# Kernel optimization log

Measured on AMD Instinct MI355X. Metric: run time of the kernel, lower is better.

The kernel has to match this reference:

```python
import jax, jax.numpy as jnp
import numpy as np

MODES = 16
WIDTH = 64
DEPTH = 4
MLP = 128


def spectral_conv(x, w_cplx):
    # x: [B, C, H, W] float32; w_cplx: [C, C, m1, m2] complex64
    B, C, H, W = x.shape
    x_ft = jnp.fft.rfft2(x)  # [B, C, H, W//2+1] complex
    m1, m2 = MODES, MODES
    low = jnp.einsum('bixy,ioxy->boxy', x_ft[:, :, :m1, :m2], w_cplx)
    out_ft = jnp.zeros((B, C, H, W // 2 + 1), dtype=jnp.complex64)
    out_ft = out_ft.at[:, :, :m1, :m2].set(low)
    return jnp.fft.irfft2(out_ft, s=(H, W)).astype(x.dtype)


def conv1x1(x, w, b):
    # x: [B,Cin,H,W], w: [Cout,Cin], b: [Cout]
    return jnp.einsum('bihw,oi->bohw', x, w) + b[None, :, None, None]


def setup_inputs() -> dict:
    key = jax.random.key(0)
    ks = jax.random.split(key, 4 + 4 * DEPTH)
    inp = {}
    inp['x'] = jax.random.normal(ks[0], (8, 3, 256, 256), dtype=jnp.float32)
    inp['fc0_w'] = jax.random.normal(ks[1], (WIDTH, 3), dtype=jnp.float32) * 0.1
    inp['fc0_b'] = jnp.zeros((WIDTH,), dtype=jnp.float32)
    scale = 1.0 / (WIDTH * WIDTH)
    sw_re, sw_im, ww, wb = [], [], [], []
    for i in range(DEPTH):
        k1, k2, k3 = jax.random.split(ks[4 + i], 3)
        sw_re.append(scale * jax.random.uniform(k1, (WIDTH, WIDTH, MODES, MODES), dtype=jnp.float32))
        sw_im.append(scale * jax.random.uniform(k2, (WIDTH, WIDTH, MODES, MODES), dtype=jnp.float32))
        ww.append(jax.random.normal(k3, (WIDTH, WIDTH), dtype=jnp.float32) * 0.05)
        wb.append(jnp.zeros((WIDTH,), dtype=jnp.float32))
    inp['spec_w_re'] = jnp.stack(sw_re)  # [D, C, C, m1, m2]
    inp['spec_w_im'] = jnp.stack(sw_im)
    inp['w_w'] = jnp.stack(ww)           # [D, C, C]
    inp['w_b'] = jnp.stack(wb)           # [D, C]
    inp['fc1_w'] = jax.random.normal(ks[2], (MLP, WIDTH), dtype=jnp.float32) * 0.05
    inp['fc1_b'] = jnp.zeros((MLP,), dtype=jnp.float32)
    inp['fc2_w'] = jax.random.normal(ks[3], (3, MLP), dtype=jnp.float32) * 0.05
    inp['fc2_b'] = jnp.zeros((3,), dtype=jnp.float32)
    return inp


def reference(x, fc0_w, fc0_b, spec_w_re, spec_w_im, w_w, w_b, fc1_w, fc1_b, fc2_w, fc2_b):
    # Dropout is identity in eval mode.
    h = conv1x1(x, fc0_w, fc0_b)  # [B, WIDTH, H, W]
    for i in range(DEPTH):
        w_cplx = spec_w_re[i] + 1j * spec_w_im[i]
        x1 = spectral_conv(h, w_cplx)
        x2 = conv1x1(h, w_w[i], w_b[i])
        h = jax.nn.relu(x1 + x2)
    h = jnp.transpose(h, (0, 2, 3, 1))  # [B, H, W, WIDTH]
    h = jax.nn.relu(jnp.einsum('bhwc,mc->bhwm', h, fc1_w) + fc1_b)
    h = jnp.einsum('bhwm,om->bhwo', h, fc2_w) + fc2_b
    return jnp.transpose(h, (0, 3, 1, 2))  # [B, 3, H, W]
```

## Files before the change

kernel.cpp:

```cpp
#include <hip/hip_runtime.h>

#define Hd 256
#define Wd 256
#define HW 65536
#define C 64
#define B 8
#define M 16
#define NDEPTH 4
#define NMLP 128

typedef __attribute__((ext_vector_type(8))) __bf16 bf16x8;
typedef __attribute__((ext_vector_type(4))) float f32x4;

__device__ inline void split_pack8(const float* v, uint4& hq, uint4& lq) {
    unsigned hw[4], lw[4];
#pragma unroll
    for (int i = 0; i < 4; ++i) {
        float a = v[2 * i], bb = v[2 * i + 1];
        unsigned ua = __float_as_uint(a);
        unsigned ha = (ua + 0x7fffu + ((ua >> 16) & 1u)) & 0xffff0000u;
        float ra = a - __uint_as_float(ha);
        unsigned ural = __float_as_uint(ra);
        unsigned la = (ural + 0x7fffu + ((ural >> 16) & 1u)) >> 16;
        unsigned ub = __float_as_uint(bb);
        unsigned hb = (ub + 0x7fffu + ((ub >> 16) & 1u)) & 0xffff0000u;
        float rb = bb - __uint_as_float(hb);
        unsigned urbl = __float_as_uint(rb);
        unsigned lb = (urbl + 0x7fffu + ((urbl >> 16) & 1u)) >> 16;
        hw[i] = (ha >> 16) | (hb & 0xffff0000u);
        lw[i] = la | (lb << 16);
    }
    hq = make_uint4(hw[0], hw[1], hw[2], hw[3]);
    lq = make_uint4(lw[0], lw[1], lw[2], lw[3]);
}

__global__ void k_table(float2* __restrict__ tab) {
    int t = threadIdx.x;
    double a = (6.283185307179586476925286766559 / 256.0) * (double)t;
    tab[t] = make_float2((float)cos(a), (float)sin(a));
}

__global__ void k_prep0(const float2* __restrict__ tab, const float* __restrict__ fc1w,
                        const float* __restrict__ ww,
                        float* __restrict__ trig, float* __restrict__ trigFT,
                        float* __restrict__ w1T, float* __restrict__ wwT_all) {
    int blk = blockIdx.x, t = threadIdx.x;
    if (blk < 32) {
        int k = blk & 15;
        float2 e = tab[(k * t) & 255];
        trig[blk * 256 + t] = (blk < 16) ? e.x : e.y;
    } else if (blk < 64) {
        int f = (blk - 32) * 256 + t;
        int y = f >> 5, kk = f & 31;
        float2 e = tab[((kk & 15) * y) & 255];
        trigFT[f] = (kk < 16) ? e.x : -e.y;
    } else if (blk < 96) {
        int f = (blk - 64) * 256 + t;
        int i = f >> 7, m = f & 127;
        w1T[f] = fc1w[m * 64 + i];
    } else {
        int f = (blk - 96) * 256 + t;
        int d = f >> 12, r = f & 4095;
        int i = r >> 6, o = r & 63;
        wwT_all[f] = ww[d * 4096 + o * 64 + i];
    }
}

__global__ void k_fc0(const float* __restrict__ x, const float* __restrict__ w,
                      const float* __restrict__ bias, float* __restrict__ h) {
    int p = blockIdx.x * 256 + threadIdx.x;
    int b = p >> 16, pix = p & 65535;
    float x0 = x[(b * 3 + 0) * HW + pix];
    float x1 = x[(b * 3 + 1) * HW + pix];
    float x2 = x[(b * 3 + 2) * HW + pix];
    for (int o = 0; o < C; ++o) {
        float v = bias[o];
        v = fmaf(w[o * 3 + 0], x0, v);
        v = fmaf(w[o * 3 + 1], x1, v);
        v = fmaf(w[o * 3 + 2], x2, v);
        h[(b * C + o) * HW + pix] = v;
    }
}

__global__ __launch_bounds__(128, 2)
void k_fwd_y(const float* __restrict__ h, const float* __restrict__ trigFT,
             float* __restrict__ T1F) {
    __shared__ float sH[32 * 256];
    __shared__ float sE[32 * 32];
    int bc = blockIdx.x, t = threadIdx.x;
    int rg = t >> 5, cg = t & 31;
    float acc[8][8];
#pragma unroll
    for (int io = 0; io < 8; ++io)
#pragma unroll
        for (int ix = 0; ix < 8; ++ix) acc[io][ix] = 0.f;
    float4* sH4 = (float4*)sH;
    float4* sE4 = (float4*)sE;
    for (int ph = 0; ph < 8; ++ph) {
#pragma unroll
        for (int p = 0; p < 16; ++p) {
            int f = t + p * 128;
            sH4[f] = *(const float4*)(h + (size_t)bc * HW + ph * 32 * 256 + f * 4);
        }
#pragma unroll
        for (int p = 0; p < 2; ++p) {
            int f = t + p * 128;
            sE4[f] = *(const float4*)(trigFT + ph * 1024 + f * 4);
        }
        __syncthreads();
#pragma unroll 4
        for (int yy = 0; yy < 32; ++yy) {
            float4 e0 = sE4[yy * 8 + rg * 2], e1 = sE4[yy * 8 + rg * 2 + 1];
            float4 h0 = sH4[yy * 64 + cg];
            float4 h1 = sH4[yy * 64 + 32 + cg];
            float ae[8] = {e0.x, e0.y, e0.z, e0.w, e1.x, e1.y, e1.z, e1.w};
            float ah[8] = {h0.x, h0.y, h0.z, h0.w, h1.x, h1.y, h1.z, h1.w};
#pragma unroll
            for (int io = 0; io < 8; ++io)
#pragma unroll
                for (int ix = 0; ix < 8; ++ix)
                    acc[io][ix] = fmaf(ae[io], ah[ix], acc[io][ix]);
        }
        __syncthreads();
    }
#pragma unroll
    for (int io = 0; io < 8; ++io) {
        float* dst = T1F + (size_t)bc * 8192 + (rg * 8 + io) * 256;
        float4 v0, v1;
        v0.x = acc[io][0]; v0.y = acc[io][1]; v0.z = acc[io][2]; v0.w = acc[io][3];
        v1.x = acc[io][4]; v1.y = acc[io][5]; v1.z = acc[io][6]; v1.w = acc[io][7];
        *(float4*)(dst + cg * 4) = v0;
        *(float4*)(dst + 128 + cg * 4) = v1;
    }
}

__global__ __launch_bounds__(256, 2)
void k_fwd_x(const float* __restrict__ T1F, const float* __restrict__ trig,
             float2* __restrict__ X) {
    __shared__ float sT[32 * 260];
    __shared__ float sG[32 * 260];
    int bc = blockIdx.x, t = threadIdx.x;
#pragma unroll
    for (int p = 0; p < 8; ++p) {
        int f = t + p * 256;
        int row = f >> 6, seg = f & 63;
        ((float4*)(sT + row * 260))[seg] = *(const float4*)(T1F + (size_t)bc * 8192 + f * 4);
        ((float4*)(sG + row * 260))[seg] = *(const float4*)(trig + row * 256 + seg * 4);
    }
    __syncthreads();
    int ky = t >> 4, kx = t & 15;
    const float* Tr = sT + ky * 260;
    const float* Ti = sT + (16 + ky) * 260;
    const float* Cs = sG + kx * 260;
    const float* Sn = sG + (16 + kx) * 260;
    float xr0 = 0.f, xi0 = 0.f, xr1 = 0.f, xi1 = 0.f;
    for (int q = 0; q < 64; q += 2) {
        float4 tr = *(const float4*)(Tr + q * 4);
        float4 ti = *(const float4*)(Ti + q * 4);
        float4 cs = *(const float4*)(Cs + q * 4);
        float4 sn = *(const float4*)(Sn + q * 4);
        xr0 = fmaf(tr.x, cs.x, xr0); xr0 = fmaf(ti.x, sn.x, xr0);
        xi0 = fmaf(ti.x, cs.x, xi0); xi0 = fmaf(-tr.x, sn.x, xi0);
        xr0 = fmaf(tr.y, cs.y, xr0); xr0 = fmaf(ti.y, sn.y, xr0);
        xi0 = fmaf(ti.y, cs.y, xi0); xi0 = fmaf(-tr.y, sn.y, xi0);
        xr0 = fmaf(tr.z, cs.z, xr0); xr0 = fmaf(ti.z, sn.z, xr0);
        xi0 = fmaf(ti.z, cs.z, xi0); xi0 = fmaf(-tr.z, sn.z, xi0);
        xr0 = fmaf(tr.w, cs.w, xr0); xr0 = fmaf(ti.w, sn.w, xr0);
        xi0 = fmaf(ti.w, cs.w, xi0); xi0 = fmaf(-tr.w, sn.w, xi0);
        float4 tr1 = *(const float4*)(Tr + q * 4 + 4);
        float4 ti1 = *(const float4*)(Ti + q * 4 + 4);
        float4 cs1 = *(const float4*)(Cs + q * 4 + 4);
        float4 sn1 = *(const float4*)(Sn + q * 4 + 4);
        xr1 = fmaf(tr1.x, cs1.x, xr1); xr1 = fmaf(ti1.x, sn1.x, xr1);
        xi1 = fmaf(ti1.x, cs1.x, xi1); xi1 = fmaf(-tr1.x, sn1.x, xi1);
        xr1 = fmaf(tr1.y, cs1.y, xr1); xr1 = fmaf(ti1.y, sn1.y, xr1);
        xi1 = fmaf(ti1.y, cs1.y, xi1); xi1 = fmaf(-tr1.y, sn1.y, xi1);
        xr1 = fmaf(tr1.z, cs1.z, xr1); xr1 = fmaf(ti1.z, sn1.z, xr1);
        xi1 = fmaf(ti1.z, cs1.z, xi1); xi1 = fmaf(-tr1.z, sn1.z, xi1);
        xr1 = fmaf(tr1.w, cs1.w, xr1); xr1 = fmaf(ti1.w, sn1.w, xr1);
        xi1 = fmaf(ti1.w, cs1.w, xi1); xi1 = fmaf(-tr1.w, sn1.w, xi1);
    }
    X[bc * 256 + t] = make_float2(xr0 + xr1, xi0 + xi1);
}

__global__ __launch_bounds__(256, 2)
void k_mix(const float2* __restrict__ X, const float* __restrict__ wre,
           const float* __restrict__ wim, float2* __restrict__ Y) {
    int o = blockIdx.x >> 2;
    int bq = blockIdx.x & 3;
    int m = threadIdx.x;
    int b0 = bq * 2, b1 = bq * 2 + 1;
    float yr0 = 0.f, yi0 = 0.f, yr1 = 0.f, yi1 = 0.f;
    for (int i = 0; i < C; ++i) {
        float wr = wre[(i * C + o) * 256 + m];
        float wi = wim[(i * C + o) * 256 + m];
        float2 x0 = X[(b0 * C + i) * 256 + m];
        float2 x1 = X[(b1 * C + i) * 256 + m];
        yr0 = fmaf(x0.x, wr, fmaf(-x0.y, wi, yr0));
        yi0 = fmaf(x0.x, wi, fmaf(x0.y, wr, yi0));
        yr1 = fmaf(x1.x, wr, fmaf(-x1.y, wi, yr1));
        yi1 = fmaf(x1.x, wi, fmaf(x1.y, wr, yi1));
    }
    Y[(b0 * C + o) * 256 + m] = make_float2(yr0, yi0);
    Y[(b1 * C + o) * 256 + m] = make_float2(yr1, yi1);
}

__global__ __launch_bounds__(256, 2)
void k_invy(const float2* __restrict__ Y, const float2* __restrict__ tab,
            float* __restrict__ Gq) {
    __shared__ float2 st[256];
    int blk = blockIdx.x;
    int yt = blk & 15, pg = (blk >> 4) & 3, b = blk >> 6;
    int t = threadIdx.x;
    st[t] = tab[t];
    int o = t & 63, kx = pg * 4 + (t >> 6);
    __syncthreads();
    float sc = (kx == 0 ? 1.0f : 2.0f) * (1.0f / 65536.0f);
    float yr[16], yi[16];
    const float2* yp = Y + (size_t)(b * 64 + o) * 256 + kx;
#pragma unroll
    for (int ky = 0; ky < 16; ++ky) {
        float2 v = yp[ky * 16];
        yr[ky] = v.x * sc;
        yi[ky] = v.y * sc;
    }
    int y0 = yt * 16;
    for (int yy = 0; yy < 16; ++yy) {
        int y = y0 + yy;
        float re = 0.f, im = 0.f;
#pragma unroll
        for (int ky = 0; ky < 16; ++ky) {
            float2 e = st[(ky * y) & 255];
            re = fmaf(yr[ky], e.x, re);
            re = fmaf(-yi[ky], e.y, re);
            im = fmaf(yr[ky], e.y, im);
            im = fmaf(yi[ky], e.x, im);
        }
        float* gp = Gq + (size_t)(b * 256 + y) * 32 * 64 + o;
        gp[kx * 64] = re;
        gp[(16 + kx) * 64] = -im;
    }
}

__global__ __launch_bounds__(256, 4)
void k_final(float* __restrict__ h, const float* __restrict__ Gq,
             const float* __restrict__ wwT, const float* __restrict__ wb,
             const float* __restrict__ trig) {
    __shared__ uint4 sHh[512], sHl[512];
    __shared__ uint4 sWh[256], sWl[256];
    int blk = blockIdx.x;
    int xq = blk & 1, y = (blk >> 1) & 255, b = blk >> 9;
    int x0 = xq * 128;
    int t = threadIdx.x;
    int xs = t & 127, half = t >> 7;
    int os = t & 63, q = t >> 6;
    int w = t >> 6, l = t & 63;
    int lr = l & 15, lq = l >> 4;
    f32x4 acc[8];
    {
        int ob = w * 16 + lq * 4;
        f32x4 ini;
        ini[0] = wb[ob]; ini[1] = wb[ob + 1]; ini[2] = wb[ob + 2]; ini[3] = wb[ob + 3];
#pragma unroll
        for (int xt = 0; xt < 8; ++xt) acc[xt] = ini;
    }
    for (int ph = 0; ph < 3; ++ph) {
        {
            const float* src; size_t str;
            if (ph < 2) {
                src = h + (size_t)(b * 64 + ph * 32 + half * 16) * HW + y * 256 + x0 + xs;
                str = HW;
            } else {
                src = trig + (half * 16) * 256 + x0 + xs;
                str = 256;
            }
            float v[16];
#pragma unroll
            for (int kk = 0; kk < 16; ++kk) v[kk] = src[(size_t)kk * str];
#pragma unroll
            for (int c2 = 0; c2 < 2; ++c2) {
                uint4 hq4, lq4;
                split_pack8(v + c2 * 8, hq4, lq4);
                int cell = (half * 2 + c2) * 128 + xs;
                sHh[cell] = hq4; sHl[cell] = lq4;
            }
        }
        {
            const float* src = (ph < 2)
                ? (wwT + (ph * 32 + q * 8) * 64 + os)
                : (Gq + ((size_t)(b * 256 + y) * 32 + q * 8) * 64 + os);
            float v[8];
#pragma unroll
            for (int kk = 0; kk < 8; ++kk) v[kk] = src[kk * 64];
            uint4 hq4, lq4;
            split_pack8(v, hq4, lq4);
            int cell = q * 64 + os;
            sWh[cell] = hq4; sWl[cell] = lq4;
        }
        __syncthreads();
        bf16x8 Ah = __builtin_bit_cast(bf16x8, sWh[lq * 64 + w * 16 + lr]);
        bf16x8 Al = __builtin_bit_cast(bf16x8, sWl[lq * 64 + w * 16 + lr]);
#pragma unroll
        for (int xt = 0; xt < 8; ++xt) {
            bf16x8 Bh = __builtin_bit_cast(bf16x8, sHh[lq * 128 + xt * 16 + lr]);
            bf16x8 Bl = __builtin_bit_cast(bf16x8, sHl[lq * 128 + xt * 16 + lr]);
            acc[xt] = __builtin_amdgcn_mfma_f32_16x16x32_bf16(Ah, Bh, acc[xt], 0, 0, 0);
            acc[xt] = __builtin_amdgcn_mfma_f32_16x16x32_bf16(Ah, Bl, acc[xt], 0, 0, 0);
            acc[xt] = __builtin_amdgcn_mfma_f32_16x16x32_bf16(Al, Bh, acc[xt], 0, 0, 0);
        }
        __syncthreads();
    }
#pragma unroll
    for (int g = 0; g < 4; ++g) {
        int o = w * 16 + lq * 4 + g;
        float* dst = h + (size_t)(b * 64 + o) * HW + y * 256 + x0 + lr;
#pragma unroll
        for (int xt = 0; xt < 8; ++xt)
            dst[xt * 16] = fmaxf(acc[xt][g], 0.f);
    }
}

__global__ __launch_bounds__(256, 3)
void k_fc12(const float* __restrict__ h, const float* __restrict__ w1T,
            const float* __restrict__ b1, const float* __restrict__ w2,
            const float* __restrict__ b2, float* __restrict__ out) {
    __shared__ uint4 sHh[512], sHl[512];
    __shared__ uint4 sWh[512], sWl[512];
    int blk = blockIdx.x;
    int xq = blk & 1, y = (blk >> 1) & 255, b = blk >> 9;
    int x0 = xq * 128;
    int t = threadIdx.x;
    int xs = t & 127, half = t >> 7;
    int w = t >> 6, l = t & 63;
    int lr = l & 15, lq = l >> 4;
    int mb = w * 32;
    f32x4 acc[2][8];
#pragma unroll
    for (int u = 0; u < 2; ++u) {
        int m0 = mb + u * 16 + lq * 4;
        f32x4 ini;
        ini[0] = b1[m0]; ini[1] = b1[m0 + 1]; ini[2] = b1[m0 + 2]; ini[3] = b1[m0 + 3];
#pragma unroll
        for (int xt = 0; xt < 8; ++xt) acc[u][xt] = ini;
    }
    for (int ph = 0; ph < 2; ++ph) {
        {
            const float* src = h + (size_t)(b * 64 + ph * 32 + half * 16) * HW + y * 256 + x0 + xs;
            float v[16];
#pragma unroll
            for (int kk = 0; kk < 16; ++kk) v[kk] = src[(size_t)kk * HW];
#pragma unroll
            for (int c2 = 0; c2 < 2; ++c2) {
                uint4 hq4, lq4;
                split_pack8(v + c2 * 8, hq4, lq4);
                int cell = (half * 2 + c2) * 128 + xs;
                sHh[cell] = hq4; sHl[cell] = lq4;
            }
        }
        {
            const float* src = w1T + (ph * 32 + half * 16) * 128 + xs;
            float v[16];
#pragma unroll
            for (int kk = 0; kk < 16; ++kk) v[kk] = src[kk * 128];
#pragma unroll
            for (int c2 = 0; c2 < 2; ++c2) {
                uint4 hq4, lq4;
                split_pack8(v + c2 * 8, hq4, lq4);
                int cell = (half * 2 + c2) * 128 + xs;
                sWh[cell] = hq4; sWl[cell] = lq4;
            }
        }
        __syncthreads();
        bf16x8 Ah[2], Al[2];
#pragma unroll
        for (int u = 0; u < 2; ++u) {
            Ah[u] = __builtin_bit_cast(bf16x8, sWh[lq * 128 + mb + u * 16 + lr]);
            Al[u] = __builtin_bit_cast(bf16x8, sWl[lq * 128 + mb + u * 16 + lr]);
        }
#pragma unroll
        for (int xt = 0; xt < 8; ++xt) {
            bf16x8 Bh = __builtin_bit_cast(bf16x8, sHh[lq * 128 + xt * 16 + lr]);
            bf16x8 Bl = __builtin_bit_cast(bf16x8, sHl[lq * 128 + xt * 16 + lr]);
#pragma unroll
            for (int u = 0; u < 2; ++u) {
                acc[u][xt] = __builtin_amdgcn_mfma_f32_16x16x32_bf16(Ah[u], Bh, acc[u][xt], 0, 0, 0);
                acc[u][xt] = __builtin_amdgcn_mfma_f32_16x16x32_bf16(Ah[u], Bl, acc[u][xt], 0, 0, 0);
                acc[u][xt] = __builtin_amdgcn_mfma_f32_16x16x32_bf16(Al[u], Bh, acc[u][xt], 0, 0, 0);
            }
        }
        __syncthreads();
    }
    float pj[3][8];
#pragma unroll
    for (int j = 0; j < 3; ++j)
#pragma unroll
        for (int xt = 0; xt < 8; ++xt) pj[j][xt] = 0.f;
#pragma unroll
    for (int u = 0; u < 2; ++u)
#pragma unroll
        for (int g = 0; g < 4; ++g) {
            int m = mb + u * 16 + lq * 4 + g;
            float w20 = w2[m], w21 = w2[NMLP + m], w22 = w2[2 * NMLP + m];
#pragma unroll
            for (int xt = 0; xt < 8; ++xt) {
                float r = fmaxf(acc[u][xt][g], 0.f);
                pj[0][xt] = fmaf(w20, r, pj[0][xt]);
                pj[1][xt] = fmaf(w21, r, pj[1][xt]);
                pj[2][xt] = fmaf(w22, r, pj[2][xt]);
            }
        }
#pragma unroll
    for (int j = 0; j < 3; ++j)
#pragma unroll
        for (int xt = 0; xt < 8; ++xt) {
            float v = pj[j][xt];
            v += __shfl_xor(v, 16);
            v += __shfl_xor(v, 32);
            pj[j][xt] = v;
        }
    float* part = (float*)sHh;
    if (lq == 0) {
#pragma unroll
        for (int j = 0; j < 3; ++j)
#pragma unroll
            for (int xt = 0; xt < 8; ++xt)
                part[(w * 3 + j) * 128 + xt * 16 + lr] = pj[j][xt];
    }
    __syncthreads();
#pragma unroll
    for (int r = 0; r < 2; ++r) {
        int idx = t + r * 256;
        if (idx < 384) {
            int j = idx >> 7, xx = idx & 127;
            float s = b2[j];
#pragma unroll
            for (int ww2 = 0; ww2 < 4; ++ww2) s += part[(ww2 * 3 + j) * 128 + xx];
            out[(size_t)(b * 3 + j) * HW + y * 256 + x0 + xx] = s;
        }
    }
}

extern "C" void kernel_launch(void* const* d_in, const int* in_sizes, int n_in,
                              void* d_out, int out_size, void* d_ws, size_t ws_size,
                              hipStream_t stream) {
    const float* x     = (const float*)d_in[0];
    const float* fc0_w = (const float*)d_in[1];
    const float* fc0_b = (const float*)d_in[2];
    const float* swre  = (const float*)d_in[3];
    const float* swim  = (const float*)d_in[4];
    const float* ww    = (const float*)d_in[5];
    const float* wb    = (const float*)d_in[6];
    const float* fc1w  = (const float*)d_in[7];
    const float* fc1b  = (const float*)d_in[8];
    const float* fc2w  = (const float*)d_in[9];
    const float* fc2b  = (const float*)d_in[10];

    float* ws = (float*)d_ws;
    float2* tab    = (float2*)ws;
    float*  h      = ws + 512;
    float*  T1F    = ws + 33554944;
    float2* X      = (float2*)(ws + 37749248);
    float2* Y      = (float2*)(ws + 38011392);
    float*  Gq     = ws + 38273536;
    float*  wwT    = ws + 42467840;
    float*  w1T    = ws + 42484224;
    float*  trig   = ws + 42492416;
    float*  trigFT = ws + 42500608;

    k_table<<<dim3(1), dim3(256), 0, stream>>>(tab);
    k_prep0<<<dim3(160), dim3(256), 0, stream>>>(tab, fc1w, ww, trig, trigFT, w1T, wwT);
    k_fc0<<<dim3(2048), dim3(256), 0, stream>>>(x, fc0_w, fc0_b, h);

    for (int d = 0; d < NDEPTH; ++d) {
        k_fwd_y<<<dim3(512), dim3(128), 0, stream>>>(h, trigFT, T1F);
        k_fwd_x<<<dim3(512), dim3(256), 0, stream>>>(T1F, trig, X);
        k_mix<<<dim3(256), dim3(256), 0, stream>>>(X, swre + (size_t)d * C * C * 256,
                                                   swim + (size_t)d * C * C * 256, Y);
        k_invy<<<dim3(512), dim3(256), 0, stream>>>(Y, tab, Gq);
        k_final<<<dim3(4096), dim3(256), 0, stream>>>(h, Gq, wwT + d * 4096, wb + d * C, trig);
    }
    k_fc12<<<dim3(4096), dim3(256), 0, stream>>>(h, w1T, fc1b, fc2w, fc2b, (float*)d_out);
}
```

Before: 706.6 us.

## Move forward y-DFT to bf16x3 split MFMA with precomputed packed trig tables

Replaces the scalar-FMA forward DFT along the height axis with a matrix-core version. Inputs and twiddles are split into hi/lo bf16 pairs and combined with three 16x16x32 bf16 MFMAs, keeping near-fp32 accuracy. A new prep kernel packs the twiddle matrix once into hi/lo bf16 tiles. Each block now covers half the row width, doubling the grid, and the new kernel adds split/pack work and strided global loads when staging h into LDS.

```diff
diff --git a/kernel.cpp b/kernel.cpp
--- a/kernel.cpp
+++ b/kernel.cpp
@@ -66,6 +66,23 @@
     }
 }
 
+__global__ void k_prep_et(const float2* __restrict__ tab,
+                          uint4* __restrict__ ETh, uint4* __restrict__ ETl) {
+    int c = blockIdx.x * 256 + threadIdx.x;
+    if (c >= 1024) return;
+    int ph = c >> 7, kc = (c >> 5) & 3, m = c & 31;
+    float v[8];
+#pragma unroll
+    for (int j = 0; j < 8; ++j) {
+        int y = ph * 32 + kc * 8 + j;
+        float2 e = tab[((m & 15) * y) & 255];
+        v[j] = (m < 16) ? e.x : -e.y;
+    }
+    uint4 hq, lq;
+    split_pack8(v, hq, lq);
+    ETh[c] = hq; ETl[c] = lq;
+}
+
 __global__ void k_fc0(const float* __restrict__ x, const float* __restrict__ w,
                       const float* __restrict__ bias, float* __restrict__ h) {
     int p = blockIdx.x * 256 + threadIdx.x;
@@ -82,56 +99,68 @@
     }
 }
 
-__global__ __launch_bounds__(128, 2)
-void k_fwd_y(const float* __restrict__ h, const float* __restrict__ trigFT,
-             float* __restrict__ T1F) {
-    __shared__ float sH[32 * 256];
-    __shared__ float sE[32 * 32];
-    int bc = blockIdx.x, t = threadIdx.x;
-    int rg = t >> 5, cg = t & 31;
-    float acc[8][8];
-#pragma unroll
-    for (int io = 0; io < 8; ++io)
-#pragma unroll
-        for (int ix = 0; ix < 8; ++ix) acc[io][ix] = 0.f;
-    float4* sH4 = (float4*)sH;
-    float4* sE4 = (float4*)sE;
+__global__ __launch_bounds__(256, 4)
+void k_fwd_y(const float* __restrict__ h, const uint4* __restrict__ ETh,
+             const uint4* __restrict__ ETl, float* __restrict__ T1F) {
+    __shared__ uint4 sBh[512], sBl[512];
+    int blk = blockIdx.x;
+    int xh = blk & 1, bc = blk >> 1;
+    int x0 = xh * 128;
+    int t = threadIdx.x;
+    int xs = t & 127, half = t >> 7;
+    int w = t >> 6, l = t & 63;
+    int lr = l & 15, lq = l >> 4;
+    f32x4 acc[2][2];
+#pragma unroll
+    for (int u = 0; u < 2; ++u)
+#pragma unroll
+        for (int xt = 0; xt < 2; ++xt) {
+            acc[u][xt][0] = 0.f; acc[u][xt][1] = 0.f;
+            acc[u][xt][2] = 0.f; acc[u][xt][3] = 0.f;
+        }
     for (int ph = 0; ph < 8; ++ph) {
-#pragma unroll
-        for (int p = 0; p < 16; ++p) {
-            int f = t + p * 128;
-            sH4[f] = *(const float4*)(h + (size_t)bc * HW + ph * 32 * 256 + f * 4);
-        }
-#pragma unroll
-        for (int p = 0; p < 2; ++p) {
-            int f = t + p * 128;
-            sE4[f] = *(const float4*)(trigFT + ph * 1024 + f * 4);
+        {
+            const float* src = h + (size_t)bc * HW + (ph * 32 + half * 16) * 256 + x0 + xs;
+            float v[16];
+#pragma unroll
+            for (int kk = 0; kk < 16; ++kk) v[kk] = src[kk * 256];
+#pragma unroll
+            for (int c2 = 0; c2 < 2; ++c2) {
+                uint4 hq4, lq4;
+                split_pack8(v + c2 * 8, hq4, lq4);
+                int cell = (half * 2 + c2) * 128 + xs;
+                sBh[cell] = hq4; sBl[cell] = lq4;
+            }
         }
         __syncthreads();
-#pragma unroll 4
-        for (int yy = 0; yy < 32; ++yy) {
-            float4 e0 = sE4[yy * 8 + rg * 2], e1 = sE4[yy * 8 + rg * 2 + 1];
-            float4 h0 = sH4[yy * 64 + cg];
-            float4 h1 = sH4[yy * 64 + 32 + cg];
-            float ae[8] = {e0.x, e0.y, e0.z, e0.w, e1.x, e1.y, e1.z, e1.w};
-            float ah[8] = {h0.x, h0.y, h0.z, h0.w, h1.x, h1.y, h1.z, h1.w};
-#pragma unroll
-            for (int io = 0; io < 8; ++io)
-#pragma unroll
-                for (int ix = 0; ix < 8; ++ix)
-                    acc[io][ix] = fmaf(ae[io], ah[ix], acc[io][ix]);
+        bf16x8 Ah[2], Al[2];
+#pragma unroll
+        for (int u = 0; u < 2; ++u) {
+            int ci = ph * 128 + lq * 32 + u * 16 + lr;
+            Ah[u] = __builtin_bit_cast(bf16x8, ETh[ci]);
+            Al[u] = __builtin_bit_cast(bf16x8, ETl[ci]);
+        }
+#pragma unroll
+        for (int xt = 0; xt < 2; ++xt) {
+            bf16x8 Bh = __builtin_bit_cast(bf16x8, sBh[lq * 128 + w * 32 + xt * 16 + lr]);
+            bf16x8 Bl = __builtin_bit_cast(bf16x8, sBl[lq * 128 + w * 32 + xt * 16 + lr]);
+#pragma unroll
+            for (int u = 0; u < 2; ++u) {
+                acc[u][xt] = __builtin_amdgcn_mfma_f32_16x16x32_bf16(Ah[u], Bh, acc[u][xt], 0, 0, 0);
+                acc[u][xt] = __builtin_amdgcn_mfma_f32_16x16x32_bf16(Ah[u], Bl, acc[u][xt], 0, 0, 0);
+                acc[u][xt] = __builtin_amdgcn_mfma_f32_16x16x32_bf16(Al[u], Bh, acc[u][xt], 0, 0, 0);
+            }
         }
         __syncthreads();
     }
 #pragma unroll
-    for (int io = 0; io < 8; ++io) {
-        float* dst = T1F + (size_t)bc * 8192 + (rg * 8 + io) * 256;
-        float4 v0, v1;
-        v0.x = acc[io][0]; v0.y = acc[io][1]; v0.z = acc[io][2]; v0.w = acc[io][3];
-        v1.x = acc[io][4]; v1.y = acc[io][5]; v1.z = acc[io][6]; v1.w = acc[io][7];
-        *(float4*)(dst + cg * 4) = v0;
-        *(float4*)(dst + 128 + cg * 4) = v1;
-    }
+    for (int u = 0; u < 2; ++u)
+#pragma unroll
+        for (int xt = 0; xt < 2; ++xt)
+#pragma unroll
+            for (int g = 0; g < 4; ++g)
+                T1F[(size_t)bc * 8192 + (u * 16 + lq * 4 + g) * 256 + x0 + w * 32 + xt * 16 + lr] =
+                    acc[u][xt][g];
 }
 
 __global__ __launch_bounds__(256, 2)
@@ -466,13 +495,16 @@
     float*  w1T    = ws + 42484224;
     float*  trig   = ws + 42492416;
     float*  trigFT = ws + 42500608;
+    uint4*  ETh    = (uint4*)(ws + 42508800);
+    uint4*  ETl    = (uint4*)(ws + 42512896);
 
     k_table<<<dim3(1), dim3(256), 0, stream>>>(tab);
     k_prep0<<<dim3(160), dim3(256), 0, stream>>>(tab, fc1w, ww, trig, trigFT, w1T, wwT);
+    k_prep_et<<<dim3(4), dim3(256), 0, stream>>>(tab, ETh, ETl);
     k_fc0<<<dim3(2048), dim3(256), 0, stream>>>(x, fc0_w, fc0_b, h);
 
     for (int d = 0; d < NDEPTH; ++d) {
-        k_fwd_y<<<dim3(512), dim3(128), 0, stream>>>(h, trigFT, T1F);
+        k_fwd_y<<<dim3(1024), dim3(256), 0, stream>>>(h, ETh, ETl, T1F);
         k_fwd_x<<<dim3(512), dim3(256), 0, stream>>>(T1F, trig, X);
         k_mix<<<dim3(256), dim3(256), 0, stream>>>(X, swre + (size_t)d * C * C * 256,
                                                    swim + (size_t)d * C * C * 256, Y);
```

After: 630.5 us. -10.8%, faster.
